# Kernel optimization log

Hardware: AMD Instinct MI355X
Metric: run time of the kernel (lower is better)

## Reference

```python
import jax, jax.numpy as jnp
import numpy as np

B, H, P, D = 32, 8, 16, 32
OUT_DIM = 32
GROUPS = 64
NUM_F = 8
N = H * P * D                 # 4096 (self.num)
PHO = P * H * OUT_DIM         # 4096


def setup_inputs() -> dict:
    key = jax.random.key(0)
    ks = jax.random.split(key, 10)
    return {
        "q": jax.random.normal(ks[0], (B, H, P, D), dtype=jnp.float32),
        "k": jax.random.normal(ks[1], (B, H, P, D), dtype=jnp.float32),
        "grid": jnp.arange(NUM_F, dtype=jnp.float32) + 1.0,
        "base_weight_q": jax.random.uniform(ks[2], (PHO, N), dtype=jnp.float32),
        "base_weight_k": jax.random.uniform(ks[3], (PHO, N), dtype=jnp.float32),
        "coef_q": jax.random.uniform(ks[4], (GROUPS, 1, NUM_F), dtype=jnp.float32),
        "coef_k": jax.random.uniform(ks[5], (GROUPS, 1, NUM_F), dtype=jnp.float32),
        # grouped 1x1 conv == num_f independent [PHO, N] matmuls (only conv_layer_q is used in forward)
        "conv_wq": jax.random.normal(ks[6], (NUM_F, PHO, N), dtype=jnp.float32) * 0.01,
        "conv_bq": jax.random.normal(ks[7], (NUM_F, PHO), dtype=jnp.float32) * 0.01,
        "scale_sp": jnp.ones((PHO,), dtype=jnp.float32),
    }


def reference(q, k, grid, base_weight_q, base_weight_k, coef_q, coef_k, conv_wq, conv_bq, scale_sp):
    b, h, p, d = q.shape
    n = h * p * d
    nf = grid.shape[0]
    gs = n // coef_q.shape[0]               # group_size
    out_dim = base_weight_q.shape[0] // (p * h)

    qf = q.reshape(b, n)
    kf = k.reshape(b, n)

    base_q = jax.nn.silu(qf) @ base_weight_q.T          # [B, PHO]
    base_k = jax.nn.silu(kf) @ base_weight_k.T

    # per-feature coef: feature i in group i//gs, scaled per frequency f -> [F, N]
    ce_q = jnp.repeat(coef_q[:, 0, :], gs, axis=0).T
    ce_k = jnp.repeat(coef_k[:, 0, :], gs, axis=0).T

    sq = jnp.sin(grid[None, :, None] * qf[:, None, :]) * ce_q[None]   # [B, F, N]
    sk = jnp.sin(grid[None, :, None] * kf[:, None, :]) * ce_k[None]

    # grouped conv1d (kernel 1, groups=num_f): per-frequency matmul; original uses conv_layer_q for both
    fq = jnp.einsum('bfn,fon->bfo', sq, conv_wq) + conv_bq[None]      # [B, F, PHO]
    fq = fq.sum(axis=1) * scale_sp
    fk = jnp.einsum('bfn,fon->bfo', sk, conv_wq) + conv_bq[None]
    fk = fk.sum(axis=1) * scale_sp

    y = (fq * scale_sp + base_q) + (fk * scale_sp + base_k)
    y = y.reshape(b, h, p, out_dim)
    return jax.nn.softmax(y, axis=-1)
```

## Files before the change

### kernel.cpp

```cpp
#include <hip/hip_runtime.h>
#include <math.h>

#define N_TOT 4096
#define PHO_T 4096
#define KTOT  40960
#define NS    2560

typedef __attribute__((ext_vector_type(8)))  short short8v;
typedef __attribute__((ext_vector_type(16))) float f32x16;

#define GLD16(src, dst) __builtin_amdgcn_global_load_lds(                      \
    (const __attribute__((address_space(1))) void*)(src),                      \
    (__attribute__((address_space(3))) void*)(dst), 16, 0, 0)

__device__ __forceinline__ void split1(float x, short& h, short& l) {
    unsigned u  = __builtin_bit_cast(unsigned, x);
    unsigned hu = (u + 0x7FFFu + ((u >> 16) & 1u)) & 0xFFFF0000u;
    h = (short)(hu >> 16);
    float r = x - __builtin_bit_cast(float, hu);
    unsigned ur = __builtin_bit_cast(unsigned, r);
    l = (short)((ur + 0x7FFFu + ((ur >> 16) & 1u)) >> 16);
}

__global__ void act_kernel(const float* __restrict__ q,
                           const float* __restrict__ kx,
                           const float* __restrict__ grid_,
                           const float* __restrict__ coefq,
                           const float* __restrict__ coefk,
                           short* __restrict__ Af)
{
    const int t = blockIdx.x * 256 + threadIdx.x;
    const int S = t >> 6;
    const int l = t & 63;
    const int b = l & 31;
    const int k0 = S * 16 + (l >> 5) * 8;

    float v[8];
    if (k0 < 8192) {
        const float* src = (k0 < 4096) ? (q  + (size_t)b * N_TOT + k0)
                                       : (kx + (size_t)b * N_TOT + (k0 - 4096));
#pragma unroll
        for (int j = 0; j < 8; ++j) {
            const float x = src[j];
            v[j] = x / (1.f + __expf(-x));
        }
    } else {
        const int f  = (k0 - 8192) >> 12;
        const int n0 = (k0 - 8192) & 4095;
        const int g  = n0 >> 6;
        const float gf  = grid_[f];
        const float cq_ = coefq[g * 8 + f];
        const float ck_ = coefk[g * 8 + f];
        const float* qp = q  + (size_t)b * N_TOT + n0;
        const float* kp = kx + (size_t)b * N_TOT + n0;
#pragma unroll
        for (int j = 0; j < 8; ++j)
            v[j] = sinf(gf * qp[j]) * cq_ + sinf(gf * kp[j]) * ck_;
    }

    short8v hi, lo;
#pragma unroll
    for (int j = 0; j < 8; ++j) { short h, lw; split1(v[j], h, lw); hi[j] = h; lo[j] = lw; }
    *(short8v*)&Af[((size_t)(S * 2 + 0) * 64 + l) * 8] = hi;
    *(short8v*)&Af[((size_t)(S * 2 + 1) * 64 + l) * 8] = lo;
}

__global__ void init_kernel(const float* __restrict__ cb,
                            const float* __restrict__ ssp,
                            float* __restrict__ ypre)
{
    const int t = blockIdx.x * 256 + threadIdx.x;
    const int o = t & 4095;
    const float s = ssp[o];
    float acc = 0.f;
#pragma unroll
    for (int f = 0; f < 8; ++f) acc += cb[f * PHO_T + o];
    ypre[t] = 2.f * s * s * acc;
}

#define OBK  256
#define KC   32
#define KSUP 1280
#define NCH  (KSUP / KC)

__global__ __launch_bounds__(256) void gemm_kernel(
    const float* __restrict__ bwq, const float* __restrict__ bwk,
    const float* __restrict__ cw,  const short* __restrict__ Af,
    const float* __restrict__ ssp, float* __restrict__ ypre)
{
    __shared__ float Wl[2][OBK * KC];

    const int t  = threadIdx.x;
    const int ks = blockIdx.x >> 4;
    const int ob = blockIdx.x & 15;
    const int o_base = ob * OBK;
    const int k_base = ks * KSUP;

    const int w  = t >> 6;
    const int l  = t & 63;
    const int srow  = l >> 3;
    const int sslot = (l & 7) ^ (srow & 7);

    f32x16 accU0, accU1, accS0, accS1;
#pragma unroll
    for (int i = 0; i < 16; ++i) {
        accU0[i] = 0.f; accU1[i] = 0.f; accS0[i] = 0.f; accS1[i] = 0.f;
    }

    auto wptr = [&](int kg) -> const float* {
        if (kg < 4096)  return bwq + kg;
        if (kg < 8192)  return bwk + (kg - 4096);
        const int f    = (kg - 8192) >> 12;
        const int noff = (kg - 8192) & 4095;
        return cw + (size_t)f * (size_t)PHO_T * N_TOT + noff;
    };

    auto stage = [&](int kg, int buf) {
        const float* Wp = wptr(kg);
#pragma unroll
        for (int i = 0; i < 8; ++i) {
            const int row = w * 64 + i * 8 + srow;
            const float* src = Wp + (size_t)(o_base + row) * N_TOT + sslot * 4;
            GLD16(src, &Wl[buf][(w * 64 + i * 8) * KC]);
        }
    };

    stage(k_base, 0);
    __syncthreads();

    const int rkey = l & 7;
    const int row0 = w * 64 + (l & 31);

    for (int c = 0; c < NCH; ++c) {
        const int cur = c & 1;
        const int kg  = k_base + c * KC;
        if (c + 1 < NCH) stage(kg + KC, cur ^ 1);

        const bool sc = (kg >= 8192);
#pragma unroll
        for (int s = 0; s < 2; ++s) {
            const size_t Sg = (size_t)(kg >> 4) + s;
            const short8v ah = *(const short8v*)&Af[((Sg * 2 + 0) * 64 + l) * 8];
            const short8v al = *(const short8v*)&Af[((Sg * 2 + 1) * 64 + l) * 8];
            const int j0 = s * 4 + (l >> 5) * 2;

            auto tileop = [&](int nt, f32x16& acc) {
                const float* rp = &Wl[cur][(row0 + nt * 32) * KC];
                const float4 wa = *(const float4*)&rp[((j0    ) ^ rkey) * 4];
                const float4 wb = *(const float4*)&rp[((j0 + 1) ^ rkey) * 4];
                short8v bh, bl;
                {
                    short h, lw;
                    split1(wa.x, h, lw); bh[0] = h; bl[0] = lw;
                    split1(wa.y, h, lw); bh[1] = h; bl[1] = lw;
                    split1(wa.z, h, lw); bh[2] = h; bl[2] = lw;
                    split1(wa.w, h, lw); bh[3] = h; bl[3] = lw;
                    split1(wb.x, h, lw); bh[4] = h; bl[4] = lw;
                    split1(wb.y, h, lw); bh[5] = h; bl[5] = lw;
                    split1(wb.z, h, lw); bh[6] = h; bl[6] = lw;
                    split1(wb.w, h, lw); bh[7] = h; bl[7] = lw;
                }
                acc = __builtin_amdgcn_mfma_f32_32x32x16_bf16(ah, bh, acc, 0, 0, 0);
                acc = __builtin_amdgcn_mfma_f32_32x32x16_bf16(ah, bl, acc, 0, 0, 0);
                acc = __builtin_amdgcn_mfma_f32_32x32x16_bf16(al, bh, acc, 0, 0, 0);
            };
            if (sc) { tileop(0, accS0); tileop(1, accS1); }
            else    { tileop(0, accU0); tileop(1, accU1); }
        }
        __syncthreads();
    }

    const int o0 = o_base + w * 64 + (l & 31);
    const int o1 = o0 + 32;
    const float x0 = ssp[o0], x1 = ssp[o1];
    const float s0 = x0 * x0, s1 = x1 * x1;
    const int bh4 = 4 * (l >> 5);
#pragma unroll
    for (int r = 0; r < 16; ++r) {
        const int b = (r & 3) + 8 * (r >> 2) + bh4;
        atomicAdd(&ypre[(size_t)b * PHO_T + o0], accU0[r] + accS0[r] * s0);
        atomicAdd(&ypre[(size_t)b * PHO_T + o1], accU1[r] + accS1[r] * s1);
    }
}

__global__ void softmax_kernel(const float* __restrict__ yp,
                               float* __restrict__ out)
{
    const int t  = threadIdx.x;
    const int r  = blockIdx.x * 8 + (t >> 5);
    const int od = t & 31;
    const float v = yp[(size_t)r * 32 + od];
    float m = v;
#pragma unroll
    for (int s = 16; s > 0; s >>= 1) m = fmaxf(m, __shfl_xor(m, s, 32));
    const float e = __expf(v - m);
    float sum = e;
#pragma unroll
    for (int s = 16; s > 0; s >>= 1) sum += __shfl_xor(sum, s, 32);
    out[(size_t)r * 32 + od] = e / sum;
}

extern "C" void kernel_launch(void* const* d_in, const int* in_sizes, int n_in,
                              void* d_out, int out_size, void* d_ws, size_t ws_size,
                              hipStream_t stream)
{
    const float* q    = (const float*)d_in[0];
    const float* k    = (const float*)d_in[1];
    const float* grid = (const float*)d_in[2];
    const float* bwq  = (const float*)d_in[3];
    const float* bwk  = (const float*)d_in[4];
    const float* cq   = (const float*)d_in[5];
    const float* ck   = (const float*)d_in[6];
    const float* cw   = (const float*)d_in[7];
    const float* cb   = (const float*)d_in[8];
    const float* ssp  = (const float*)d_in[9];
    float* out = (float*)d_out;

    short* Af   = (short*)d_ws;
    float* ypre = (float*)((char*)d_ws + (size_t)NS * 2 * 64 * 16);

    act_kernel<<<640, 256, 0, stream>>>(q, k, grid, cq, ck, Af);
    init_kernel<<<512, 256, 0, stream>>>(cb, ssp, ypre);
    gemm_kernel<<<512, 256, 0, stream>>>(bwq, bwk, cw, Af, ssp, ypre);
    softmax_kernel<<<512, 256, 0, stream>>>(ypre, out);
}
```

Measured before the change: 160.9 us.

## Drop block barriers in GEMM loop using per-wave LDS staging and explicit vmcnt waits

Each wave stages into and reads from only its own 64-row slice of the LDS weight tile, so the GEMM main loop replaces __syncthreads with explicit s_waitcnt vmcnt waits. The activation fragments are now loaded before the next stage is issued, and the last chunk is peeled to wait on all loads. This is meant to remove block-wide barrier stalls and let waves run independently to keep more memory traffic in flight. Separately, the sin terms in the activation kernel switch to the fast __sinf intrinsic, which is cheaper but less accurate for large arguments (grid up to 8 times normal inputs).

```diff
diff --git a/kernel.cpp b/kernel.cpp
--- a/kernel.cpp
+++ b/kernel.cpp
@@ -55,7 +55,7 @@
         const float* kp = kx + (size_t)b * N_TOT + n0;
 #pragma unroll
         for (int j = 0; j < 8; ++j)
-            v[j] = sinf(gf * qp[j]) * cq_ + sinf(gf * kp[j]) * ck_;
+            v[j] = __sinf(gf * qp[j]) * cq_ + __sinf(gf * kp[j]) * ck_;
     }
 
     short8v hi, lo;
@@ -125,24 +125,18 @@
         }
     };
 
-    stage(k_base, 0);
-    __syncthreads();
-
     const int rkey = l & 7;
     const int row0 = w * 64 + (l & 31);
-
-    for (int c = 0; c < NCH; ++c) {
-        const int cur = c & 1;
-        const int kg  = k_base + c * KC;
-        if (c + 1 < NCH) stage(kg + KC, cur ^ 1);
-
+    const int j0b  = (l >> 5) * 2;
+
+    auto compute = [&](int kg, int cur, const short8v& ah0, const short8v& al0,
+                       const short8v& ah1, const short8v& al1) {
         const bool sc = (kg >= 8192);
 #pragma unroll
         for (int s = 0; s < 2; ++s) {
-            const size_t Sg = (size_t)(kg >> 4) + s;
-            const short8v ah = *(const short8v*)&Af[((Sg * 2 + 0) * 64 + l) * 8];
-            const short8v al = *(const short8v*)&Af[((Sg * 2 + 1) * 64 + l) * 8];
-            const int j0 = s * 4 + (l >> 5) * 2;
+            const short8v& ah = s ? ah1 : ah0;
+            const short8v& al = s ? al1 : al0;
+            const int j0 = s * 4 + j0b;
 
             auto tileop = [&](int nt, f32x16& acc) {
                 const float* rp = &Wl[cur][(row0 + nt * 32) * KC];
@@ -167,7 +161,36 @@
             if (sc) { tileop(0, accS0); tileop(1, accS1); }
             else    { tileop(0, accU0); tileop(1, accU1); }
         }
-        __syncthreads();
+    };
+
+    stage(k_base, 0);
+
+    short8v ah0, al0, ah1, al1;
+    for (int c = 0; c < NCH - 1; ++c) {
+        const int cur = c & 1;
+        const int kg  = k_base + c * KC;
+        const size_t Sg = (size_t)(kg >> 4);
+        ah0 = *(const short8v*)&Af[(((Sg    ) * 2 + 0) * 64 + l) * 8];
+        al0 = *(const short8v*)&Af[(((Sg    ) * 2 + 1) * 64 + l) * 8];
+        ah1 = *(const short8v*)&Af[(((Sg + 1) * 2 + 0) * 64 + l) * 8];
+        al1 = *(const short8v*)&Af[(((Sg + 1) * 2 + 1) * 64 + l) * 8];
+        asm volatile("" ::: "memory");
+        stage(kg + KC, cur ^ 1);
+        asm volatile("s_waitcnt vmcnt(8)" ::: "memory");
+        __builtin_amdgcn_sched_barrier(0);
+        compute(kg, cur, ah0, al0, ah1, al1);
+    }
+    {
+        const int c   = NCH - 1;
+        const int kg  = k_base + c * KC;
+        const size_t Sg = (size_t)(kg >> 4);
+        ah0 = *(const short8v*)&Af[(((Sg    ) * 2 + 0) * 64 + l) * 8];
+        al0 = *(const short8v*)&Af[(((Sg    ) * 2 + 1) * 64 + l) * 8];
+        ah1 = *(const short8v*)&Af[(((Sg + 1) * 2 + 0) * 64 + l) * 8];
+        al1 = *(const short8v*)&Af[(((Sg + 1) * 2 + 1) * 64 + l) * 8];
+        asm volatile("s_waitcnt vmcnt(0)" ::: "memory");
+        __builtin_amdgcn_sched_barrier(0);
+        compute(kg, c & 1, ah0, al0, ah1, al1);
     }
 
     const int o0 = o_base + w * 64 + (l & 31);
```

After: 142.6 us. 1.13x faster.
